# Optimization experiments

Hardware: AMD Instinct MI355X
Metric: run time of the kernel (lower is better)

The kernel has to match this reference:

```python
import jax, jax.numpy as jnp
import numpy as np

C = 256          # C_in == C_out
G = C // 4       # groups = C_in/4 -> 4 channels per group
K = 3
STRIDE = 1
PAD = 2
DIL = 2
EPS = 1e-5

@jax.custom_vjp
def binarize(x):
    # 1-bit sign binarization with straight-through estimator (STE)
    return jnp.sign(x)

def _bin_fwd(x):
    return jnp.sign(x), x

def _bin_bwd(x, g):
    # STE with hardtanh clip: pass grad where |x| <= 1
    return (g * (jnp.abs(x) <= 1.0).astype(g.dtype),)

binarize.defvjp(_bin_fwd, _bin_bwd)

def setup_inputs() -> dict:
    key = jax.random.key(0)
    k1, k2, k3, k4, k5, k6 = jax.random.split(key, 6)
    x = jax.random.normal(k1, (64, C, 32, 32), jnp.float32)
    # grouped conv weight: [C_out, C_in/groups, K, K] = [256, 4, 3, 3]
    weight = jax.random.normal(k2, (C, C // G, K, K), jnp.float32) * 0.1
    gamma = 1.0 + 0.1 * jax.random.normal(k3, (C,), jnp.float32)
    beta = 0.1 * jax.random.normal(k4, (C,), jnp.float32)
    running_mean = 0.1 * jax.random.normal(k5, (C,), jnp.float32)
    running_var = jax.random.uniform(k6, (C,), jnp.float32, 0.5, 1.5)
    return {"x": x, "weight": weight, "gamma": gamma, "beta": beta,
            "running_mean": running_mean, "running_var": running_var}

def reference(x, weight, gamma, beta, running_mean, running_var):
    # BatchNorm2d (inference form with running stats)
    inv = gamma * jax.lax.rsqrt(running_var + EPS)            # [C]
    h = x * inv[None, :, None, None] + (beta - running_mean * inv)[None, :, None, None]
    # binarize activations and weights (1w1a)
    a = binarize(h)
    w = binarize(weight)
    # grouped dilated conv, stride 1, pad 2, dilation 2 -> same HxW
    out = jax.lax.conv_general_dilated(
        a, w,
        window_strides=(STRIDE, STRIDE),
        padding=[(PAD, PAD), (PAD, PAD)],
        rhs_dilation=(DIL, DIL),
        dimension_numbers=("NCHW", "OIHW", "NCHW"),
        feature_group_count=G)
    # channel shuffle: [N,C,H,W] -> [N,g,C/g,H,W] -> [N,C/g,g,H,W] -> [N,C,H,W]
    N, Cc, H, W = out.shape
    out = out.reshape(N, G, Cc // G, H, W).transpose(0, 2, 1, 3, 4).reshape(N, Cc, H, W)
    # identity shortcut (stride == 1)
    return out + x
```

## Files before the change

kernel.cpp:

```cpp
#include <hip/hip_runtime.h>

#ifndef __has_builtin
#define __has_builtin(x) 0
#endif

#if __has_builtin(__builtin_amdgcn_sdot4)
#define DOT4(a, b, c) __builtin_amdgcn_sdot4((a), (b), (c), false)
#else
__device__ __forceinline__ int dot4_sw(int a, int b, int c) {
#pragma unroll
    for (int k = 0; k < 4; ++k)
        c += (int)(signed char)((a >> (8 * k)) & 0xff) *
             (int)(signed char)((b >> (8 * k)) & 0xff);
    return c;
}
#define DOT4(a, b, c) dot4_sw((a), (b), (c))
#endif

constexpr int CH   = 256;
constexpr int NPIX = 1024;
constexpr int LW   = 33;
constexpr float BN_EPS = 1e-5f;

__device__ __forceinline__ float rfl_f(float v) {
    return __int_as_float(__builtin_amdgcn_readfirstlane(__float_as_int(v)));
}

__global__ __launch_bounds__(256, 4)
void bconv(const float* __restrict__ x,
           const float* __restrict__ wgt,
           const float* __restrict__ gamma,
           const float* __restrict__ beta,
           const float* __restrict__ rmean,
           const float* __restrict__ rvar,
           float* __restrict__ out) {
    __shared__ int   pk_lds[2][32][LW];
    __shared__ int   wq_lds[36];
    __shared__ float bn_lds[8];

    const int tid  = threadIdx.x;
    const int n0   = (blockIdx.x >> 6) * 2;
    const int g    = blockIdx.x & 63;
    const int pix0 = tid * 4;
    const int row  = pix0 >> 5;
    const int col0 = pix0 & 31;
    const float* xnA = x + n0 * CH * NPIX;
    const float* xnB = xnA + CH * NPIX;
    float* onA = out + n0 * CH * NPIX;
    float* onB = onA + CH * NPIX;

    float4 xvA[4], scA[4], xvB[4], scB[4];
#pragma unroll
    for (int ci = 0; ci < 4; ++ci)
        xvA[ci] = *(const float4*)(xnA + (g * 4 + ci) * NPIX + pix0);
#pragma unroll
    for (int c2 = 0; c2 < 4; ++c2)
        scA[c2] = *(const float4*)(xnA + (c2 * 64 + g) * NPIX + pix0);
#pragma unroll
    for (int ci = 0; ci < 4; ++ci)
        xvB[ci] = *(const float4*)(xnB + (g * 4 + ci) * NPIX + pix0);
#pragma unroll
    for (int c2 = 0; c2 < 4; ++c2)
        scB[c2] = *(const float4*)(xnB + (c2 * 64 + g) * NPIX + pix0);

    if (tid < 144) {
        const int c2 = tid / 36, r = tid % 36, ci = r / 9, tap = r % 9;
        float w = wgt[g * 144 + tid];
        int s = (w > 0.f) ? 1 : ((w < 0.f) ? -1 : 0);
        ((char*)wq_lds)[(c2 * 9 + tap) * 4 + ci] = (char)s;
    } else if (tid < 148) {
        const int ci = tid - 144, c = g * 4 + ci;
        float r  = __fdiv_rn(1.0f, __fsqrt_rn(__fadd_rn(rvar[c], BN_EPS)));
        float iv = __fmul_rn(gamma[c], r);
        bn_lds[ci]     = iv;
        bn_lds[4 + ci] = __fsub_rn(beta[c], __fmul_rn(rmean[c], iv));
    }

    float inv[4], bias[4];
#pragma unroll
    for (int ci = 0; ci < 4; ++ci) {
        const int c = g * 4 + ci;
        float r  = __fdiv_rn(1.0f, __fsqrt_rn(__fadd_rn(rvar[c], BN_EPS)));
        inv[ci]  = __fmul_rn(gamma[c], r);
        bias[ci] = __fsub_rn(beta[c], __fmul_rn(rmean[c], inv[ci]));
    }

    auto pack_to_lds = [&](const float4 xv[4], int img) {
#pragma unroll
        for (int p = 0; p < 4; ++p) {
            int v = 0;
#pragma unroll
            for (int ci = 0; ci < 4; ++ci) {
                float h = __fadd_rn(__fmul_rn(((const float*)&xv[ci])[p], inv[ci]), bias[ci]);
                int s = (h > 0.f) ? 1 : ((h < 0.f) ? -1 : 0);
                v |= (s & 0xff) << (8 * ci);
            }
            pk_lds[img][row][col0 + p] = v;
        }
    };

    pack_to_lds(xvA, 0);
    __syncthreads();

    int wq[4][9];
#pragma unroll
    for (int c2 = 0; c2 < 4; ++c2)
#pragma unroll
        for (int t = 0; t < 9; ++t)
            wq[c2][t] = __builtin_amdgcn_readfirstlane(wq_lds[c2 * 9 + t]);

    const bool le = (col0 == 0), re = (col0 == 28);

    auto gather = [&](int img, int a[3][8]) {
#pragma unroll
        for (int kh = 0; kh < 3; ++kh) {
            const int rs  = row + 2 * kh - 2;
            const int rr  = min(max(rs, 0), 31);
            const bool okr = (unsigned)rs < 32u;
#pragma unroll
            for (int j = 0; j < 8; ++j) {
                const int c  = col0 - 2 + j;
                const int cc = min(max(c, 0), 31);
                const bool okc = !(j < 2 && le) && !(j > 5 && re);
                int v = pk_lds[img][rr][cc];
                a[kh][j] = (okr && okc) ? v : 0;
            }
        }
    };

    auto compute = [&](const int a[3][8], const float4 sc[4], float4 o[4]) {
#pragma unroll
        for (int c2 = 0; c2 < 4; ++c2)
#pragma unroll
            for (int p = 0; p < 4; ++p) {
                int acc = 0;
#pragma unroll
                for (int kh = 0; kh < 3; ++kh)
#pragma unroll
                    for (int kw = 0; kw < 3; ++kw)
                        acc = DOT4(a[kh][p + 2 * kw], wq[c2][kh * 3 + kw], acc);
                ((float*)&o[c2])[p] = __fadd_rn((float)acc, ((const float*)&sc[c2])[p]);
            }
    };

    int aA[3][8];
    gather(0, aA);
    float4 oA[4];
    compute(aA, scA, oA);

    pack_to_lds(xvB, 1);
    __syncthreads();

#pragma unroll
    for (int c2 = 0; c2 < 4; ++c2)
        *(float4*)(onA + (c2 * 64 + g) * NPIX + pix0) = oA[c2];

    int aB[3][8];
    gather(1, aB);
    float4 oB[4];
    compute(aB, scB, oB);
#pragma unroll
    for (int c2 = 0; c2 < 4; ++c2)
        *(float4*)(onB + (c2 * 64 + g) * NPIX + pix0) = oB[c2];
}

extern "C" void kernel_launch(void* const* d_in, const int* in_sizes, int n_in,
                              void* d_out, int out_size, void* d_ws, size_t ws_size,
                              hipStream_t stream) {
    const float* x     = (const float*)d_in[0];
    const float* wgt   = (const float*)d_in[1];
    const float* gamma = (const float*)d_in[2];
    const float* beta  = (const float*)d_in[3];
    const float* rmean = (const float*)d_in[4];
    const float* rvar  = (const float*)d_in[5];
    float* out = (float*)d_out;

    const int N = in_sizes[0] / (CH * NPIX);
    bconv<<<(N / 2) * 64, 256, 0, stream>>>(x, wgt, gamma, beta, rmean, rvar, out);
}
```

Measured before the change: 34.95 us.

## Use zero-padded LDS tiles with vector gathers, per-thread weight packing, single barrier

Adds a 2-element zero halo around each packed activation tile in LDS. Each tap row can then be gathered with two int4 loads, with no clamping or edge masks. Each thread now packs the binarized weights directly from global memory (same address across threads), replacing the LDS staging and readfirstlane. Both images are packed before a single barrier, and the shortcut loads are deferred until just before use, which lowers register pressure at the cost of less early latency hiding.

```diff
diff --git a/kernel.cpp b/kernel.cpp
--- a/kernel.cpp
+++ b/kernel.cpp
@@ -19,12 +19,9 @@
 
 constexpr int CH   = 256;
 constexpr int NPIX = 1024;
-constexpr int LW   = 33;
+constexpr int PR   = 36;
+constexpr int PC   = 40;
 constexpr float BN_EPS = 1e-5f;
-
-__device__ __forceinline__ float rfl_f(float v) {
-    return __int_as_float(__builtin_amdgcn_readfirstlane(__float_as_int(v)));
-}
 
 __global__ __launch_bounds__(256, 4)
 void bconv(const float* __restrict__ x,
@@ -34,9 +31,7 @@
            const float* __restrict__ rmean,
            const float* __restrict__ rvar,
            float* __restrict__ out) {
-    __shared__ int   pk_lds[2][32][LW];
-    __shared__ int   wq_lds[36];
-    __shared__ float bn_lds[8];
+    __shared__ __align__(16) int pk_lds[2][PR][PC];
 
     const int tid  = threadIdx.x;
     const int n0   = (blockIdx.x >> 6) * 2;
@@ -49,32 +44,45 @@
     float* onA = out + n0 * CH * NPIX;
     float* onB = onA + CH * NPIX;
 
-    float4 xvA[4], scA[4], xvB[4], scB[4];
+    float4 xvA[4], xvB[4];
 #pragma unroll
     for (int ci = 0; ci < 4; ++ci)
         xvA[ci] = *(const float4*)(xnA + (g * 4 + ci) * NPIX + pix0);
 #pragma unroll
-    for (int c2 = 0; c2 < 4; ++c2)
-        scA[c2] = *(const float4*)(xnA + (c2 * 64 + g) * NPIX + pix0);
-#pragma unroll
     for (int ci = 0; ci < 4; ++ci)
         xvB[ci] = *(const float4*)(xnB + (g * 4 + ci) * NPIX + pix0);
+
+    {
+        int* f0 = &pk_lds[0][0][0];
+        int* f1 = &pk_lds[1][0][0];
+        if (tid < 80) {
+            f0[tid] = 0; f0[34 * PC + tid] = 0;
+            f1[tid] = 0; f1[34 * PC + tid] = 0;
+        }
+        if (tid < 128) {
+            const int r = 2 + (tid >> 2);
+            const int c = ((tid & 2) ? 34 : 0) + (tid & 1);
+            pk_lds[0][r][c] = 0;
+            pk_lds[1][r][c] = 0;
+        }
+    }
+
+    const int* wb = (const int*)(wgt + g * 144);
+    int wq[4][9];
 #pragma unroll
     for (int c2 = 0; c2 < 4; ++c2)
-        scB[c2] = *(const float4*)(xnB + (c2 * 64 + g) * NPIX + pix0);
-
-    if (tid < 144) {
-        const int c2 = tid / 36, r = tid % 36, ci = r / 9, tap = r % 9;
-        float w = wgt[g * 144 + tid];
-        int s = (w > 0.f) ? 1 : ((w < 0.f) ? -1 : 0);
-        ((char*)wq_lds)[(c2 * 9 + tap) * 4 + ci] = (char)s;
-    } else if (tid < 148) {
-        const int ci = tid - 144, c = g * 4 + ci;
-        float r  = __fdiv_rn(1.0f, __fsqrt_rn(__fadd_rn(rvar[c], BN_EPS)));
-        float iv = __fmul_rn(gamma[c], r);
-        bn_lds[ci]     = iv;
-        bn_lds[4 + ci] = __fsub_rn(beta[c], __fmul_rn(rmean[c], iv));
-    }
+#pragma unroll
+        for (int t = 0; t < 9; ++t) {
+            int pk = 0;
+#pragma unroll
+            for (int ci = 0; ci < 4; ++ci) {
+                const int b = wb[c2 * 36 + ci * 9 + t];
+                const int mag = b & 0x7fffffff;
+                const int s = (mag == 0) ? 0 : ((b < 0) ? -1 : 1);
+                pk |= (s & 0xff) << (8 * ci);
+            }
+            wq[c2][t] = pk;
+        }
 
     float inv[4], bias[4];
 #pragma unroll
@@ -95,39 +103,23 @@
                 int s = (h > 0.f) ? 1 : ((h < 0.f) ? -1 : 0);
                 v |= (s & 0xff) << (8 * ci);
             }
-            pk_lds[img][row][col0 + p] = v;
+            pk_lds[img][row + 2][col0 + 2 + p] = v;
         }
     };
+    pack_to_lds(xvA, 0);
+    pack_to_lds(xvB, 1);
 
-    pack_to_lds(xvA, 0);
     __syncthreads();
-
-    int wq[4][9];
-#pragma unroll
-    for (int c2 = 0; c2 < 4; ++c2)
-#pragma unroll
-        for (int t = 0; t < 9; ++t)
-            wq[c2][t] = __builtin_amdgcn_readfirstlane(wq_lds[c2 * 9 + t]);
-
-    const bool le = (col0 == 0), re = (col0 == 28);
 
     auto gather = [&](int img, int a[3][8]) {
 #pragma unroll
         for (int kh = 0; kh < 3; ++kh) {
-            const int rs  = row + 2 * kh - 2;
-            const int rr  = min(max(rs, 0), 31);
-            const bool okr = (unsigned)rs < 32u;
-#pragma unroll
-            for (int j = 0; j < 8; ++j) {
-                const int c  = col0 - 2 + j;
-                const int cc = min(max(c, 0), 31);
-                const bool okc = !(j < 2 && le) && !(j > 5 && re);
-                int v = pk_lds[img][rr][cc];
-                a[kh][j] = (okr && okc) ? v : 0;
-            }
+            const int4 lo = *(const int4*)&pk_lds[img][row + 2 * kh][col0];
+            const int4 hi = *(const int4*)&pk_lds[img][row + 2 * kh][col0 + 4];
+            a[kh][0] = lo.x; a[kh][1] = lo.y; a[kh][2] = lo.z; a[kh][3] = lo.w;
+            a[kh][4] = hi.x; a[kh][5] = hi.y; a[kh][6] = hi.z; a[kh][7] = hi.w;
         }
     };
-
     auto compute = [&](const int a[3][8], const float4 sc[4], float4 o[4]) {
 #pragma unroll
         for (int c2 = 0; c2 < 4; ++c2)
@@ -143,18 +135,22 @@
             }
     };
 
+    float4 scA[4];
+#pragma unroll
+    for (int c2 = 0; c2 < 4; ++c2)
+        scA[c2] = *(const float4*)(xnA + (c2 * 64 + g) * NPIX + pix0);
     int aA[3][8];
     gather(0, aA);
     float4 oA[4];
     compute(aA, scA, oA);
-
-    pack_to_lds(xvB, 1);
-    __syncthreads();
-
 #pragma unroll
     for (int c2 = 0; c2 < 4; ++c2)
         *(float4*)(onA + (c2 * 64 + g) * NPIX + pix0) = oA[c2];
 
+    float4 scB[4];
+#pragma unroll
+    for (int c2 = 0; c2 < 4; ++c2)
+        scB[c2] = *(const float4*)(xnB + (c2 * 64 + g) * NPIX + pix0);
     int aB[3][8];
     gather(1, aB);
     float4 oB[4];
```

After: 36.23 us. 3.6% more time.
